# Kernel tuning notes

Measured on AMD Instinct MI355X. Metric: run time of the kernel, lower is better.

Reference implementation:

```python
import jax, jax.numpy as jnp
import numpy as np

N_NODES = 50000
N_EDGES = 1_600_000
N_GRAPHS = 2048
NEG_SLOPE = 0.2


def setup_inputs() -> dict:
    key = jax.random.key(0)
    ks = jax.random.split(key, 24)
    p = {}
    p["x1"] = jax.random.normal(ks[0], (N_NODES, 7), jnp.float32)
    p["x2"] = jax.random.normal(ks[1], (N_NODES, 7), jnp.float32)
    p["edge_index1"] = jax.random.randint(ks[2], (2, N_EDGES), 0, N_NODES, jnp.int32)
    p["edge_index2"] = jax.random.randint(ks[3], (2, N_EDGES), 0, N_NODES, jnp.int32)
    p["batch"] = jnp.sort(jax.random.randint(ks[4], (N_NODES,), 0, N_GRAPHS, jnp.int32))
    p["half_y"] = jax.random.randint(ks[5], (N_GRAPHS,), 0, 3, jnp.int32)
    p["x_norm2_1"] = jax.random.normal(ks[6], (N_GRAPHS, 16), jnp.float32)
    p["x_norm2_2"] = jax.random.normal(ks[7], (N_GRAPHS, 16), jnp.float32)
    # GATConv params: W [in,out] (no bias in lin), att_src/att_dst [out], bias [out]
    dims = [(7, 128), (128, 128), (128, 64)]
    ki = 8
    for i, (din, dout) in enumerate(dims, start=1):
        s = 1.0 / np.sqrt(din)
        p[f"W{i}"] = jax.random.normal(ks[ki], (din, dout), jnp.float32) * s; ki += 1
        p[f"as{i}"] = jax.random.normal(ks[ki], (dout,), jnp.float32) * 0.1; ki += 1
        p[f"ad{i}"] = jax.random.normal(ks[ki], (dout,), jnp.float32) * 0.1; ki += 1
        p[f"b{i}"] = jnp.zeros((dout,), jnp.float32)
    p["linW"] = jax.random.normal(ks[ki], (64 + 16, 64), jnp.float32) * (1.0 / np.sqrt(80.0)); ki += 1
    p["linb"] = jnp.zeros((64,), jnp.float32)
    return p


def gat_conv(x, src, dst, W, a_src, a_dst, bias):
    # PyG GATConv, heads=1: h = x@W; e_{j->i} = leaky_relu(a_src.h_j + a_dst.h_i);
    # softmax over incoming edges at dst; out_i = sum_j alpha * h_j + bias
    n = x.shape[0]
    h = x @ W                              # [N, out]
    al_s = h @ a_src                       # [N]
    al_d = h @ a_dst                       # [N]
    e = jax.nn.leaky_relu(al_s[src] + al_d[dst], NEG_SLOPE)  # [E]
    m = jax.ops.segment_max(e, dst, num_segments=n)
    ex = jnp.exp(e - m[dst])
    den = jax.ops.segment_sum(ex, dst, num_segments=n)
    alpha = ex / den[dst]
    out = jax.ops.segment_sum(alpha[:, None] * h[src], dst, num_segments=n)
    return out + bias


def branch(x, edge_index, convs):
    n = x.shape[0]
    loop = jnp.arange(n, dtype=edge_index.dtype)
    src = jnp.concatenate([edge_index[0], loop])  # add_self_loops=True
    dst = jnp.concatenate([edge_index[1], loop])
    for (W, a_s, a_d, b) in convs:
        x = jax.nn.elu(gat_conv(x, src, dst, W, a_s, a_d, b))
        # dropout p=0.5 is identity in eval mode
    return x


def global_mean_pool(x, batch, num_graphs):
    sums = jax.ops.segment_sum(x, batch, num_segments=num_graphs)
    cnt = jax.ops.segment_sum(jnp.ones((x.shape[0],), x.dtype), batch, num_segments=num_graphs)
    return sums / jnp.maximum(cnt, 1.0)[:, None]


def reference(x1, x2, edge_index1, edge_index2, batch, half_y, x_norm2_1, x_norm2_2,
              W1, as1, ad1, b1, W2, as2, ad2, b2, W3, as3, ad3, b3, linW, linb):
    convs = [(W1, as1, ad1, b1), (W2, as2, ad2, b2), (W3, as3, ad3, b3)]
    h1 = branch(x1, edge_index1, convs)
    h2 = branch(x2, edge_index2, convs)
    g1 = global_mean_pool(h1, batch, N_GRAPHS)
    g2 = global_mean_pool(h2, batch, N_GRAPHS)
    g1 = jnp.concatenate([g1, x_norm2_1], axis=1)
    g2 = jnp.concatenate([g2, x_norm2_2], axis=1)
    o1 = g1 @ linW + linb
    o2 = g2 @ linW + linb
    return (o1, o2)
```

## Files before the change

### kernel.cpp

```cpp
#include <hip/hip_runtime.h>
#include <math.h>

#define N_NODES_C 50000
#define N_EDGES_C 1600000
#define N_GRAPHS_C 2048
#define NBUK 391

typedef short short8 __attribute__((ext_vector_type(8)));
typedef float f32x4 __attribute__((ext_vector_type(4)));

static __device__ __forceinline__ int lowerBound(const int* __restrict__ a, int n, int v) {
    int lo = 0, hi = n;
    while (lo < hi) {
        int mid = (lo + hi) >> 1;
        if (a[mid] < v) lo = mid + 1; else hi = mid;
    }
    return lo;
}

static __device__ __forceinline__ unsigned short f2bf(float f) {
    unsigned u = __float_as_uint(f);
    return (unsigned short)((u + 0x7FFFu + ((u >> 16) & 1u)) >> 16);
}
static __device__ __forceinline__ float blo(unsigned v) { return __uint_as_float(v << 16); }
static __device__ __forceinline__ float bhi(unsigned v) { return __uint_as_float(v & 0xFFFF0000u); }


__global__ __launch_bounds__(256) void bucket_count_kernel(
    const int* __restrict__ ei, int* __restrict__ bucketCnt, int E) {
    __shared__ int lh[NBUK];
    int t = threadIdx.x;
    for (int i = t; i < NBUK; i += 256) lh[i] = 0;
    __syncthreads();
    for (int e = blockIdx.x * blockDim.x + t; e < E; e += gridDim.x * blockDim.x)
        atomicAdd(&lh[((unsigned)ei[E + e]) >> 7], 1);
    __syncthreads();
    for (int i = t; i < NBUK; i += 256) {
        int c = lh[i];
        if (c) atomicAdd(&bucketCnt[i], c);
    }
}

__global__ __launch_bounds__(512) void bucket_scan_kernel(
    const int* __restrict__ bucketCnt, int* __restrict__ bucketPtr, int* __restrict__ bucketCur) {
    __shared__ int v[512];
    int t = threadIdx.x;
    int x = (t < NBUK) ? bucketCnt[t] : 0;
    v[t] = x;
    __syncthreads();
    for (int off = 1; off < 512; off <<= 1) {
        int y = (t >= off) ? v[t - off] : 0;
        __syncthreads();
        v[t] += y;
        __syncthreads();
    }
    int excl = v[t] - x;
    if (t <= NBUK) bucketPtr[t] = excl;
    if (t < NBUK) bucketCur[t] = excl;
}

__global__ __launch_bounds__(256) void bucket_scatter_kernel(
    const int* __restrict__ ei, int* __restrict__ bucketCur,
    unsigned* __restrict__ bucketBuf, int E) {
    __shared__ int lh[NBUK];
    int t = threadIdx.x;
    for (int i = t; i < NBUK; i += 256) lh[i] = 0;
    __syncthreads();
    int per = (E + gridDim.x - 1) / gridDim.x;
    int beg = blockIdx.x * per;
    int end = min(beg + per, E);
    for (int e = beg + t; e < end; e += 256)
        atomicAdd(&lh[((unsigned)ei[E + e]) >> 7], 1);
    __syncthreads();
    for (int i = t; i < NBUK; i += 256) {
        int c = lh[i];
        lh[i] = c ? atomicAdd(&bucketCur[i], c) : 0;
    }
    __syncthreads();
    for (int e = beg + t; e < end; e += 256) {
        int s = ei[e], d = ei[E + e];
        int pos = atomicAdd(&lh[((unsigned)d) >> 7], 1);
        bucketBuf[pos] = (unsigned)s | ((unsigned)(d & 127) << 16);
    }
}

__global__ __launch_bounds__(256) void csr_finalize_kernel(
    const int* __restrict__ bucketPtr, const unsigned* __restrict__ bucketBuf,
    int* __restrict__ rowptr, int* __restrict__ csr, int n) {
    __shared__ int hist[128], sc[128], cur[128];
    int b = blockIdx.x, t = threadIdx.x;
    int base = b << 7;
    int nb = min(128, n - base);
    if (t < 128) hist[t] = (t < nb) ? 1 : 0;
    __syncthreads();
    int ebeg = bucketPtr[b], eend = bucketPtr[b + 1];
    for (int i = ebeg + t; i < eend; i += 256)
        atomicAdd(&hist[bucketBuf[i] >> 16], 1);
    __syncthreads();
    if (t < 128) sc[t] = hist[t];
    __syncthreads();
    for (int off = 1; off < 128; off <<= 1) {
        int y = 0;
        if (t < 128 && t >= off) y = sc[t - off];
        __syncthreads();
        if (t < 128) sc[t] += y;
        __syncthreads();
    }
    int csrStart = ebeg + base;
    if (t < nb) {
        int rpos = csrStart + sc[t] - hist[t];
        rowptr[base + t] = rpos;
        csr[rpos] = base + t;
        cur[t] = rpos + 1;
    }
    if (b == 0 && t == 0) rowptr[n] = bucketPtr[NBUK] + n;
    __syncthreads();
    for (int i = ebeg + t; i < eend; i += 256) {
        unsigned v = bucketBuf[i];
        int pos = atomicAdd(&cur[v >> 16], 1);
        csr[pos] = (int)(v & 0xFFFFu);
    }
}


__global__ __launch_bounds__(256) void wt_conv_kernel(
    const float* __restrict__ W, unsigned short* __restrict__ Wt, int K, int C) {
    int i = blockIdx.x * 256 + threadIdx.x;
    if (i < K * C) {
        int c = i / K, k = i - c * K;
        Wt[i] = f2bf(W[(size_t)k * C + c]);
    }
}


template<int DOUT>
__global__ __launch_bounds__(256) void gemm_mfma(
    const unsigned short* __restrict__ xb,
    const unsigned short* __restrict__ Wt,
    const float* __restrict__ avs, const float* __restrict__ avd,
    unsigned* __restrict__ hb,
    float* __restrict__ als, float* __restrict__ ald, int n) {
    constexpr int NT = DOUT / 16;
    int w = threadIdx.x >> 6, l = threadIdx.x & 63;
    int lc = l & 15, lg = l >> 4;
    int n0 = blockIdx.x * 64 + w * 16;
    int nrow = min(n0 + lc, n - 1);
    f32x4 acc[NT];
#pragma unroll
    for (int ct = 0; ct < NT; ct++) acc[ct] = (f32x4){0.f, 0.f, 0.f, 0.f};
    const unsigned short* xrow = xb + (size_t)nrow * 128 + lg * 8;
#pragma unroll
    for (int kb = 0; kb < 128; kb += 32) {
        short8 xf = *(const short8*)(xrow + kb);
#pragma unroll
        for (int ct = 0; ct < NT; ct++) {
            short8 wf = *(const short8*)(Wt + (size_t)(ct * 16 + lc) * 128 + kb + lg * 8);
            acc[ct] = __builtin_amdgcn_mfma_f32_16x16x32_bf16(wf, xf, acc[ct], 0, 0, 0);
        }
    }
    int node = n0 + lc;
    bool ok = node < n;
    float ps = 0.f, pd = 0.f;
#pragma unroll
    for (int ct = 0; ct < NT; ct++) {
        int cb = ct * 16 + lg * 4;
#pragma unroll
        for (int j = 0; j < 4; j++) { ps += acc[ct][j] * avs[cb + j]; pd += acc[ct][j] * avd[cb + j]; }
        if (ok) {
            uint2 v;
            v.x = (unsigned)f2bf(acc[ct][0]) | ((unsigned)f2bf(acc[ct][1]) << 16);
            v.y = (unsigned)f2bf(acc[ct][2]) | ((unsigned)f2bf(acc[ct][3]) << 16);
            *(uint2*)&hb[(size_t)node * (DOUT / 2) + ct * 8 + lg * 2] = v;
        }
    }
    ps += __shfl_xor(ps, 16); ps += __shfl_xor(ps, 32);
    pd += __shfl_xor(pd, 16); pd += __shfl_xor(pd, 32);
    if (ok && lg == 0) { als[node] = ps; ald[node] = pd; }
}


__global__ __launch_bounds__(256) void linear_att_l1(
    const float* __restrict__ x, const float* __restrict__ W,
    const float* __restrict__ avs, const float* __restrict__ avd,
    unsigned* __restrict__ hb, float* __restrict__ als, float* __restrict__ ald, int n) {
    __shared__ float Wl[7 * 128];
    __shared__ float xsh[32][8];
    int tid = threadIdx.x;
    for (int i = tid; i < 7 * 128; i += 256) Wl[i] = W[i];
    int nodeBase = blockIdx.x * 32;
    if (tid < 224) {
        int nd = tid / 7, k = tid % 7;
        int g = min(nodeBase + nd, n - 1);
        xsh[nd][k] = x[(size_t)g * 7 + k];
    }
    __syncthreads();
    int nl = tid >> 3;
    int og = (tid & 7) * 16;
    int g = nodeBase + nl;
    float acc[16];
#pragma unroll
    for (int o = 0; o < 16; o++) acc[o] = 0.f;
#pragma unroll
    for (int k = 0; k < 7; k++) {
        float xv = xsh[nl][k];
#pragma unroll
        for (int o = 0; o < 16; o++) acc[o] += xv * Wl[k * 128 + og + o];
    }
    if (g < n) {
        unsigned pk[8];
#pragma unroll
        for (int o = 0; o < 16; o += 2)
            pk[o >> 1] = (unsigned)f2bf(acc[o]) | ((unsigned)f2bf(acc[o + 1]) << 16);
        uint4 v0, v1;
        v0.x = pk[0]; v0.y = pk[1]; v0.z = pk[2]; v0.w = pk[3];
        v1.x = pk[4]; v1.y = pk[5]; v1.z = pk[6]; v1.w = pk[7];
        *(uint4*)&hb[(size_t)g * 64 + (og >> 1)] = v0;
        *(uint4*)&hb[(size_t)g * 64 + (og >> 1) + 4] = v1;
        float ps = 0.f, pd = 0.f;
#pragma unroll
        for (int o = 0; o < 16; o++) { ps += acc[o] * avs[og + o]; pd += acc[o] * avd[og + o]; }
#pragma unroll
        for (int off = 1; off < 8; off <<= 1) { ps += __shfl_xor(ps, off); pd += __shfl_xor(pd, off); }
        if ((tid & 7) == 0) { als[g] = ps; ald[g] = pd; }
    }
}


template<int DOUT, bool OBF>
__global__ __launch_bounds__(256) void gat_agg3(
    const int* __restrict__ rowptr, const int* __restrict__ csr,
    const float* __restrict__ als, const float* __restrict__ ald,
    const unsigned* __restrict__ hb, const float* __restrict__ bias,
    float* __restrict__ xout, int n) {
    constexpr int RSU = DOUT / 2;
    __shared__ int   s_src[4][64];
    __shared__ float s_alpha[4][64];
    __shared__ float s_ms[4][2];
    int tid = threadIdx.x;
    int w = tid >> 6, lane = tid & 63;
    int node = min(blockIdx.x * 4 + w, n - 1);
    int beg = rowptr[node], end = rowptr[node + 1];
    int deg = end - beg, lim = min(deg, 64);
    float adi = ald[node];

    float m = -INFINITY, s = 0.f;
    int src0 = 0; float e0 = -INFINITY;
    for (int idx = beg + lane; idx < end; idx += 64) {
        int src = csr[idx];
        float e = als[src] + adi;
        e = (e > 0.f) ? e : 0.2f * e;
        if (idx == beg + lane) { src0 = src; e0 = e; }
        if (e > m) { s *= expf(m - e); m = e; }
        s += expf(e - m);
    }
#pragma unroll
    for (int o = 1; o < 64; o <<= 1) {
        float m2 = __shfl_xor(m, o);
        float s2 = __shfl_xor(s, o);
        float M = fmaxf(m, m2);
        float t1 = (m == M) ? s : s * expf(m - M);
        float t2 = (m2 == M) ? s2 : s2 * expf(m2 - M);
        m = M; s = t1 + t2;
    }
    float inv_den = 1.f / s;
    s_src[w][lane] = src0;
    s_alpha[w][lane] = (lane < lim) ? expf(e0 - m) * inv_den : 0.f;
    if (lane == 0) { s_ms[w][0] = m; s_ms[w][1] = inv_den; }
    __syncthreads();

    float accx = 0.f, accy = 0.f;
    if constexpr (DOUT == 128) {
        int j = 0;
        for (; j + 4 <= lim; j += 4) {
            int i0 = s_src[w][j], i1 = s_src[w][j + 1], i2 = s_src[w][j + 2], i3 = s_src[w][j + 3];
            float a0 = s_alpha[w][j], a1 = s_alpha[w][j + 1], a2 = s_alpha[w][j + 2], a3 = s_alpha[w][j + 3];
            unsigned v0 = hb[(size_t)i0 * RSU + lane];
            unsigned v1 = hb[(size_t)i1 * RSU + lane];
            unsigned v2 = hb[(size_t)i2 * RSU + lane];
            unsigned v3 = hb[(size_t)i3 * RSU + lane];
            accx += a0 * blo(v0) + a1 * blo(v1) + a2 * blo(v2) + a3 * blo(v3);
            accy += a0 * bhi(v0) + a1 * bhi(v1) + a2 * bhi(v2) + a3 * bhi(v3);
        }
        for (; j < lim; j++) {
            unsigned v = hb[(size_t)s_src[w][j] * RSU + lane];
            float a = s_alpha[w][j];
            accx += a * blo(v); accy += a * bhi(v);
        }
        if (deg > 64) {
            float mm = s_ms[w][0], iv = s_ms[w][1];
            for (int idx = beg + 64; idx < end; idx++) {
                int src = csr[idx];
                float e = als[src] + adi;
                e = (e > 0.f) ? e : 0.2f * e;
                float a = expf(e - mm) * iv;
                unsigned v = hb[(size_t)src * RSU + lane];
                accx += a * blo(v); accy += a * bhi(v);
            }
        }
        int c0 = lane * 2;
        float vx = accx + bias[c0], vy = accy + bias[c0 + 1];
        vx = (vx > 0.f) ? vx : expm1f(vx);
        vy = (vy > 0.f) ? vy : expm1f(vy);
        if constexpr (OBF) {
            ((unsigned*)xout)[(size_t)node * 64 + lane] =
                (unsigned)f2bf(vx) | ((unsigned)f2bf(vy) << 16);
        } else {
            *(float2*)&xout[(size_t)node * 128 + c0] = make_float2(vx, vy);
        }
    } else {
        int half = lane >> 5, lcol = lane & 31;
        int limUp = (lim + 3) & ~3;
        for (int j = 0; j < limUp; j += 4) {
            int je0 = j + half, je1 = j + 2 + half;
            int i0 = s_src[w][je0], i1 = s_src[w][je1];
            float a0 = s_alpha[w][je0], a1 = s_alpha[w][je1];
            unsigned v0 = hb[(size_t)i0 * RSU + lcol];
            unsigned v1 = hb[(size_t)i1 * RSU + lcol];
            accx += a0 * blo(v0) + a1 * blo(v1);
            accy += a0 * bhi(v0) + a1 * bhi(v1);
        }
        if (deg > 64) {
            float mm = s_ms[w][0], iv = s_ms[w][1];
            for (int idx = beg + 64; idx < end; idx++) {
                int src = csr[idx];
                float e = als[src] + adi;
                e = (e > 0.f) ? e : 0.2f * e;
                float a = expf(e - mm) * iv;
                if (half == 0) {
                    unsigned v = hb[(size_t)src * RSU + lcol];
                    accx += a * blo(v); accy += a * bhi(v);
                }
            }
        }
        accx += __shfl_xor(accx, 32);
        accy += __shfl_xor(accy, 32);
        if (half == 0) {
            int c0 = lcol * 2;
            float vx = accx + bias[c0], vy = accy + bias[c0 + 1];
            vx = (vx > 0.f) ? vx : expm1f(vx);
            vy = (vy > 0.f) ? vy : expm1f(vy);
            if constexpr (OBF) {
                ((unsigned*)xout)[(size_t)node * 32 + lcol] =
                    (unsigned)f2bf(vx) | ((unsigned)f2bf(vy) << 16);
            } else {
                *(float2*)&xout[(size_t)node * 64 + c0] = make_float2(vx, vy);
            }
        }
    }
}


__global__ __launch_bounds__(64) void pool_final_kernel(
    const float* __restrict__ x, const int* __restrict__ batch,
    const float* __restrict__ xnorm, const float* __restrict__ linW,
    const float* __restrict__ linb, float* __restrict__ out, int n) {
    int g = blockIdx.x, t = threadIdx.x;
    int lo = lowerBound(batch, n, g);
    int hi = lowerBound(batch, n, g + 1);
    float sum = 0.f;
    for (int i = lo; i < hi; i++) sum += x[(size_t)i * 64 + t];
    float cnt = (float)(hi - lo);
    float mean = sum / fmaxf(cnt, 1.f);
    __shared__ float gv[80];
    gv[t] = mean;
    if (t < 16) gv[64 + t] = xnorm[g * 16 + t];
    __syncthreads();
    float acc = linb[t];
#pragma unroll
    for (int k = 0; k < 80; k++) acc += gv[k] * linW[k * 64 + t];
    out[(size_t)g * 64 + t] = acc;
}


extern "C" void kernel_launch(void* const* d_in, const int* in_sizes, int n_in,
                              void* d_out, int out_size, void* d_ws, size_t ws_size,
                              hipStream_t stream) {
    const float* x1  = (const float*)d_in[0];
    const float* x2  = (const float*)d_in[1];
    const int*   ei1 = (const int*)d_in[2];
    const int*   ei2 = (const int*)d_in[3];
    const int*   batch = (const int*)d_in[4];
    const float* xn1 = (const float*)d_in[6];
    const float* xn2 = (const float*)d_in[7];
    const float* W1 = (const float*)d_in[8];
    const float* as1 = (const float*)d_in[9];
    const float* ad1 = (const float*)d_in[10];
    const float* b1 = (const float*)d_in[11];
    const float* W2 = (const float*)d_in[12];
    const float* as2 = (const float*)d_in[13];
    const float* ad2 = (const float*)d_in[14];
    const float* b2 = (const float*)d_in[15];
    const float* W3 = (const float*)d_in[16];
    const float* as3 = (const float*)d_in[17];
    const float* ad3 = (const float*)d_in[18];
    const float* b3 = (const float*)d_in[19];
    const float* linW = (const float*)d_in[20];
    const float* linb = (const float*)d_in[21];
    float* out = (float*)d_out;

    char* ws = (char*)d_ws;
    size_t off = 0;
    auto alloc = [&](size_t bytes) -> void* {
        void* p = ws + off;
        off += (bytes + 255) & ~(size_t)255;
        return p;
    };
    int* rowptr    = (int*)alloc((N_NODES_C + 1) * sizeof(int));
    int* csr       = (int*)alloc((size_t)(N_EDGES_C + N_NODES_C) * sizeof(int));
    float* als     = (float*)alloc(N_NODES_C * sizeof(float));
    float* ald     = (float*)alloc(N_NODES_C * sizeof(float));
    int* bucketCnt = (int*)alloc(NBUK * sizeof(int));
    int* bucketPtr = (int*)alloc((NBUK + 1) * sizeof(int));
    int* bucketCur = (int*)alloc(NBUK * sizeof(int));
    unsigned short* Wt2 = (unsigned short*)alloc(128 * 128 * sizeof(unsigned short));
    unsigned short* Wt3 = (unsigned short*)alloc(64 * 128 * sizeof(unsigned short));
    float* bufX    = (float*)alloc((size_t)N_NODES_C * 64 * sizeof(float));
    unsigned* hb   = (unsigned*)alloc((size_t)N_NODES_C * 64 * sizeof(unsigned));
    unsigned short* xbb = (unsigned short*)alloc((size_t)N_NODES_C * 128 * sizeof(unsigned short));
    unsigned* bucketBuf = (unsigned*)bufX;
    (void)ws_size; (void)in_sizes; (void)n_in; (void)out_size;

    const int GEMM_GRID = (N_NODES_C + 63) / 64;
    const int AGG_GRID = (N_NODES_C + 3) / 4;

    wt_conv_kernel<<<(128 * 128 + 255) / 256, 256, 0, stream>>>(W2, Wt2, 128, 128);
    wt_conv_kernel<<<(128 * 64 + 255) / 256, 256, 0, stream>>>(W3, Wt3, 128, 64);

    for (int br = 0; br < 2; br++) {
        const float* x  = (br == 0) ? x1 : x2;
        const int*   ei = (br == 0) ? ei1 : ei2;
        const float* xn = (br == 0) ? xn1 : xn2;
        float* o = out + (size_t)br * N_GRAPHS_C * 64;

        hipMemsetAsync(bucketCnt, 0, NBUK * sizeof(int), stream);
        bucket_count_kernel<<<1024, 256, 0, stream>>>(ei, bucketCnt, N_EDGES_C);
        bucket_scan_kernel<<<1, 512, 0, stream>>>(bucketCnt, bucketPtr, bucketCur);
        bucket_scatter_kernel<<<256, 256, 0, stream>>>(ei, bucketCur, bucketBuf, N_EDGES_C);
        csr_finalize_kernel<<<NBUK, 256, 0, stream>>>(bucketPtr, bucketBuf, rowptr, csr, N_NODES_C);

        linear_att_l1<<<(N_NODES_C + 31) / 32, 256, 0, stream>>>(x, W1, as1, ad1, hb, als, ald, N_NODES_C);
        gat_agg3<128, true><<<AGG_GRID, 256, 0, stream>>>(rowptr, csr, als, ald, hb, b1, (float*)xbb, N_NODES_C);
        gemm_mfma<128><<<GEMM_GRID, 256, 0, stream>>>(xbb, Wt2, as2, ad2, hb, als, ald, N_NODES_C);
        gat_agg3<128, true><<<AGG_GRID, 256, 0, stream>>>(rowptr, csr, als, ald, hb, b2, (float*)xbb, N_NODES_C);
        gemm_mfma<64><<<GEMM_GRID, 256, 0, stream>>>(xbb, Wt3, as3, ad3, hb, als, ald, N_NODES_C);
        gat_agg3<64, false><<<AGG_GRID, 256, 0, stream>>>(rowptr, csr, als, ald, hb, b3, bufX, N_NODES_C);

        pool_final_kernel<<<N_GRAPHS_C, 64, 0, stream>>>(bufX, batch, xn, linW, linb, o, N_NODES_C);
    }
}
```

Measured before the change: 618.6 us.

## Rewrite GAT aggregation with 16-byte gathers, shuffles and two-pass softmax

Replaces the aggregation kernel with one wave per block, one node per wave. Lanes gather 16-byte chunks of neighbor rows, so several edges are processed in parallel per instruction, with a lane-group reduction at the end. Source indices and alpha weights travel by wave shuffles instead of shared memory and __syncthreads. Softmax now takes a max pass and then a sum pass instead of the online rescaling version. The aim is fewer, wider memory transactions and more loads in flight per edge. The cost is a cross-lane reduction of eight accumulators and 64-thread blocks, which may limit occupancy.

Measured after the change: 646.4 us. 4.5% more time.

```diff
diff --git a/kernel.cpp b/kernel.cpp
--- a/kernel.cpp
+++ b/kernel.cpp
@@ -227,124 +227,128 @@
 
 
 template<int DOUT, bool OBF>
-__global__ __launch_bounds__(256) void gat_agg3(
+__global__ __launch_bounds__(64) void gat_agg4(
     const int* __restrict__ rowptr, const int* __restrict__ csr,
     const float* __restrict__ als, const float* __restrict__ ald,
-    const unsigned* __restrict__ hb, const float* __restrict__ bias,
+    const unsigned char* __restrict__ hbB, const float* __restrict__ bias,
     float* __restrict__ xout, int n) {
-    constexpr int RSU = DOUT / 2;
-    __shared__ int   s_src[4][64];
-    __shared__ float s_alpha[4][64];
-    __shared__ float s_ms[4][2];
-    int tid = threadIdx.x;
-    int w = tid >> 6, lane = tid & 63;
-    int node = min(blockIdx.x * 4 + w, n - 1);
+    constexpr int ROWB = DOUT * 2;
+    constexpr int LPE  = ROWB / 16;
+    constexpr int EPG  = 64 / LPE;
+    int lane = threadIdx.x;
+    int node = blockIdx.x;
+    if (node >= n) return;
     int beg = rowptr[node], end = rowptr[node + 1];
-    int deg = end - beg, lim = min(deg, 64);
+    int deg = end - beg;
     float adi = ald[node];
 
-    float m = -INFINITY, s = 0.f;
-    int src0 = 0; float e0 = -INFINITY;
-    for (int idx = beg + lane; idx < end; idx += 64) {
-        int src = csr[idx];
-        float e = als[src] + adi;
-        e = (e > 0.f) ? e : 0.2f * e;
-        if (idx == beg + lane) { src0 = src; e0 = e; }
-        if (e > m) { s *= expf(m - e); m = e; }
-        s += expf(e - m);
-    }
-#pragma unroll
-    for (int o = 1; o < 64; o <<= 1) {
-        float m2 = __shfl_xor(m, o);
-        float s2 = __shfl_xor(s, o);
-        float M = fmaxf(m, m2);
-        float t1 = (m == M) ? s : s * expf(m - M);
-        float t2 = (m2 == M) ? s2 : s2 * expf(m2 - M);
-        m = M; s = t1 + t2;
-    }
+    float e0 = -INFINITY, mloc = -INFINITY;
+    int src0 = node;
+    {
+        int idx = beg + lane;
+        if (idx < end) {
+            int src = csr[idx];
+            float e = als[src] + adi;
+            e = (e > 0.f) ? e : 0.2f * e;
+            e0 = e; mloc = e; src0 = src;
+            for (idx += 64; idx < end; idx += 64) {
+                src = csr[idx];
+                e = als[src] + adi;
+                e = (e > 0.f) ? e : 0.2f * e;
+                mloc = fmaxf(mloc, e);
+            }
+        }
+    }
+#pragma unroll
+    for (int o = 1; o < 64; o <<= 1) mloc = fmaxf(mloc, __shfl_xor(mloc, o));
+    float m = mloc;
+    float p0 = expf(e0 - m);
+    float sloc = p0;
+    if (deg > 64) {
+        for (int idx = beg + lane + 64; idx < end; idx += 64) {
+            int src = csr[idx];
+            float e = als[src] + adi;
+            e = (e > 0.f) ? e : 0.2f * e;
+            sloc += expf(e - m);
+        }
+    }
+    float s = sloc;
+#pragma unroll
+    for (int o = 1; o < 64; o <<= 1) s += __shfl_xor(s, o);
     float inv_den = 1.f / s;
-    s_src[w][lane] = src0;
-    s_alpha[w][lane] = (lane < lim) ? expf(e0 - m) * inv_den : 0.f;
-    if (lane == 0) { s_ms[w][0] = m; s_ms[w][1] = inv_den; }
-    __syncthreads();
-
-    float accx = 0.f, accy = 0.f;
-    if constexpr (DOUT == 128) {
-        int j = 0;
-        for (; j + 4 <= lim; j += 4) {
-            int i0 = s_src[w][j], i1 = s_src[w][j + 1], i2 = s_src[w][j + 2], i3 = s_src[w][j + 3];
-            float a0 = s_alpha[w][j], a1 = s_alpha[w][j + 1], a2 = s_alpha[w][j + 2], a3 = s_alpha[w][j + 3];
-            unsigned v0 = hb[(size_t)i0 * RSU + lane];
-            unsigned v1 = hb[(size_t)i1 * RSU + lane];
-            unsigned v2 = hb[(size_t)i2 * RSU + lane];
-            unsigned v3 = hb[(size_t)i3 * RSU + lane];
-            accx += a0 * blo(v0) + a1 * blo(v1) + a2 * blo(v2) + a3 * blo(v3);
-            accy += a0 * bhi(v0) + a1 * bhi(v1) + a2 * bhi(v2) + a3 * bhi(v3);
-        }
-        for (; j < lim; j++) {
-            unsigned v = hb[(size_t)s_src[w][j] * RSU + lane];
-            float a = s_alpha[w][j];
-            accx += a * blo(v); accy += a * bhi(v);
-        }
-        if (deg > 64) {
-            float mm = s_ms[w][0], iv = s_ms[w][1];
-            for (int idx = beg + 64; idx < end; idx++) {
+
+    int eSel = lane / LPE;
+    const unsigned char* hbs = hbB + (lane % LPE) * 16;
+    unsigned ownOff = (unsigned)node * ROWB;
+
+    float acc[8];
+#pragma unroll
+    for (int i = 0; i < 8; i++) acc[i] = 0.f;
+
+    for (int win = 0; win < deg; win += 64) {
+        float alphaL; unsigned offL;
+        if (win == 0) {
+            alphaL = p0 * inv_den;
+            offL = (beg + lane < end) ? (unsigned)src0 * ROWB : ownOff;
+        } else {
+            int idx = beg + win + lane;
+            if (idx < end) {
                 int src = csr[idx];
                 float e = als[src] + adi;
                 e = (e > 0.f) ? e : 0.2f * e;
-                float a = expf(e - mm) * iv;
-                unsigned v = hb[(size_t)src * RSU + lane];
-                accx += a * blo(v); accy += a * bhi(v);
-            }
-        }
-        int c0 = lane * 2;
-        float vx = accx + bias[c0], vy = accy + bias[c0 + 1];
-        vx = (vx > 0.f) ? vx : expm1f(vx);
-        vy = (vy > 0.f) ? vy : expm1f(vy);
+                alphaL = expf(e - m) * inv_den;
+                offL = (unsigned)src * ROWB;
+            } else { alphaL = 0.f; offL = ownOff; }
+        }
+        int limW = min(deg - win, 64);
+        int nG = (limW + EPG - 1) / EPG;
+        unsigned off_c = (unsigned)__shfl((int)offL, eSel);
+        float a_c = __shfl(alphaL, eSel);
+        uint4 v_c = *(const uint4*)(hbs + off_c);
+        for (int g = 1; g < nG; g++) {
+            int slot = g * EPG + eSel;
+            unsigned off_n = (unsigned)__shfl((int)offL, slot);
+            float a_n = __shfl(alphaL, slot);
+            uint4 v_n = *(const uint4*)(hbs + off_n);
+            acc[0] += a_c * blo(v_c.x); acc[1] += a_c * bhi(v_c.x);
+            acc[2] += a_c * blo(v_c.y); acc[3] += a_c * bhi(v_c.y);
+            acc[4] += a_c * blo(v_c.z); acc[5] += a_c * bhi(v_c.z);
+            acc[6] += a_c * blo(v_c.w); acc[7] += a_c * bhi(v_c.w);
+            off_c = off_n; a_c = a_n; v_c = v_n;
+        }
+        acc[0] += a_c * blo(v_c.x); acc[1] += a_c * bhi(v_c.x);
+        acc[2] += a_c * blo(v_c.y); acc[3] += a_c * bhi(v_c.y);
+        acc[4] += a_c * blo(v_c.z); acc[5] += a_c * bhi(v_c.z);
+        acc[6] += a_c * blo(v_c.w); acc[7] += a_c * bhi(v_c.w);
+    }
+
+#pragma unroll
+    for (int o = LPE; o < 64; o <<= 1) {
+#pragma unroll
+        for (int i = 0; i < 8; i++) acc[i] += __shfl_xor(acc[i], o);
+    }
+
+    if (lane < LPE) {
+        int c0 = lane * 8;
+        float v[8];
+#pragma unroll
+        for (int i = 0; i < 8; i++) {
+            float t = acc[i] + bias[c0 + i];
+            v[i] = (t > 0.f) ? t : expm1f(t);
+        }
         if constexpr (OBF) {
-            ((unsigned*)xout)[(size_t)node * 64 + lane] =
-                (unsigned)f2bf(vx) | ((unsigned)f2bf(vy) << 16);
+            uint4 pk;
+            pk.x = (unsigned)f2bf(v[0]) | ((unsigned)f2bf(v[1]) << 16);
+            pk.y = (unsigned)f2bf(v[2]) | ((unsigned)f2bf(v[3]) << 16);
+            pk.z = (unsigned)f2bf(v[4]) | ((unsigned)f2bf(v[5]) << 16);
+            pk.w = (unsigned)f2bf(v[6]) | ((unsigned)f2bf(v[7]) << 16);
+            *(uint4*)((unsigned*)xout + (size_t)node * (DOUT / 2) + lane * 4) = pk;
         } else {
-            *(float2*)&xout[(size_t)node * 128 + c0] = make_float2(vx, vy);
-        }
-    } else {
-        int half = lane >> 5, lcol = lane & 31;
-        int limUp = (lim + 3) & ~3;
-        for (int j = 0; j < limUp; j += 4) {
-            int je0 = j + half, je1 = j + 2 + half;
-            int i0 = s_src[w][je0], i1 = s_src[w][je1];
-            float a0 = s_alpha[w][je0], a1 = s_alpha[w][je1];
-            unsigned v0 = hb[(size_t)i0 * RSU + lcol];
-            unsigned v1 = hb[(size_t)i1 * RSU + lcol];
-            accx += a0 * blo(v0) + a1 * blo(v1);
-            accy += a0 * bhi(v0) + a1 * bhi(v1);
-        }
-        if (deg > 64) {
-            float mm = s_ms[w][0], iv = s_ms[w][1];
-            for (int idx = beg + 64; idx < end; idx++) {
-                int src = csr[idx];
-                float e = als[src] + adi;
-                e = (e > 0.f) ? e : 0.2f * e;
-                float a = expf(e - mm) * iv;
-                if (half == 0) {
-                    unsigned v = hb[(size_t)src * RSU + lcol];
-                    accx += a * blo(v); accy += a * bhi(v);
-                }
-            }
-        }
-        accx += __shfl_xor(accx, 32);
-        accy += __shfl_xor(accy, 32);
-        if (half == 0) {
-            int c0 = lcol * 2;
-            float vx = accx + bias[c0], vy = accy + bias[c0 + 1];
-            vx = (vx > 0.f) ? vx : expm1f(vx);
-            vy = (vy > 0.f) ? vy : expm1f(vy);
-            if constexpr (OBF) {
-                ((unsigned*)xout)[(size_t)node * 32 + lcol] =
-                    (unsigned)f2bf(vx) | ((unsigned)f2bf(vy) << 16);
-            } else {
-                *(float2*)&xout[(size_t)node * 64 + c0] = make_float2(vx, vy);
-            }
+            float4 f0, f1;
+            f0.x = v[0]; f0.y = v[1]; f0.z = v[2]; f0.w = v[3];
+            f1.x = v[4]; f1.y = v[5]; f1.z = v[6]; f1.w = v[7];
+            *(float4*)&xout[(size_t)node * DOUT + c0] = f0;
+            *(float4*)&xout[(size_t)node * DOUT + c0 + 4] = f1;
         }
     }
 }
@@ -421,7 +425,6 @@
     (void)ws_size; (void)in_sizes; (void)n_in; (void)out_size;
 
     const int GEMM_GRID = (N_NODES_C + 63) / 64;
-    const int AGG_GRID = (N_NODES_C + 3) / 4;
 
     wt_conv_kernel<<<(128 * 128 + 255) / 256, 256, 0, stream>>>(W2, Wt2, 128, 128);
     wt_conv_kernel<<<(128 * 64 + 255) / 256, 256, 0, stream>>>(W3, Wt3, 128, 64);
@@ -439,11 +442,11 @@
         csr_finalize_kernel<<<NBUK, 256, 0, stream>>>(bucketPtr, bucketBuf, rowptr, csr, N_NODES_C);
 
         linear_att_l1<<<(N_NODES_C + 31) / 32, 256, 0, stream>>>(x, W1, as1, ad1, hb, als, ald, N_NODES_C);
-        gat_agg3<128, true><<<AGG_GRID, 256, 0, stream>>>(rowptr, csr, als, ald, hb, b1, (float*)xbb, N_NODES_C);
+        gat_agg4<128, true><<<N_NODES_C, 64, 0, stream>>>(rowptr, csr, als, ald, (const unsigned char*)hb, b1, (float*)xbb, N_NODES_C);
         gemm_mfma<128><<<GEMM_GRID, 256, 0, stream>>>(xbb, Wt2, as2, ad2, hb, als, ald, N_NODES_C);
-        gat_agg3<128, true><<<AGG_GRID, 256, 0, stream>>>(rowptr, csr, als, ald, hb, b2, (float*)xbb, N_NODES_C);
+        gat_agg4<128, true><<<N_NODES_C, 64, 0, stream>>>(rowptr, csr, als, ald, (const unsigned char*)hb, b2, (float*)xbb, N_NODES_C);
         gemm_mfma<64><<<GEMM_GRID, 256, 0, stream>>>(xbb, Wt3, as3, ad3, hb, als, ald, N_NODES_C);
-        gat_agg3<64, false><<<AGG_GRID, 256, 0, stream>>>(rowptr, csr, als, ald, hb, b3, bufX, N_NODES_C);
+        gat_agg4<64, false><<<N_NODES_C, 64, 0, stream>>>(rowptr, csr, als, ald, (const unsigned char*)hb, b3, bufX, N_NODES_C);
 
         pool_final_kernel<<<N_GRAPHS_C, 64, 0, stream>>>(bufX, batch, xn, linW, linb, o, N_NODES_C);
     }
```
